# Performance work log

Measured on AMD Instinct MI355X. Metric: run time of the kernel, lower is better.

The kernel has to match this reference:

```python
import jax, jax.numpy as jnp
import numpy as np

H, W = 512, 512
CHUNK = 128            # gaussians blended per scan step
BLUR = 0.3             # antialiasing dilation (as in 3DGS EWA low-pass)
ALPHA_MIN = 1.0 / 255.0
ALPHA_MAX = 0.99


def setup_inputs() -> dict:
    key = jax.random.key(0)
    k = jax.random.split(key, 6)
    N = 8192
    means2D = jax.random.uniform(k[0], (N, 2), jnp.float32) * jnp.array([W, H], jnp.float32)
    colors = jax.random.uniform(k[1], (N, 3), jnp.float32)
    opacities = jax.random.uniform(k[2], (N, 1), jnp.float32)
    scales = jax.random.uniform(k[3], (N, 2), jnp.float32) * 15.0 + 1.0   # pixels
    rotations = jax.random.uniform(k[4], (N, 1), jnp.float32) * (2.0 * np.pi)
    depths = jax.random.uniform(k[5], (N,), jnp.float32)
    background = jnp.zeros((3,), jnp.float32)
    return dict(means2D=means2D, colors=colors, opacities=opacities,
                scales=scales, rotations=rotations, depths=depths,
                background=background)


def _rasterize(means2D, colors, opacities, scales, rotations, depths, background):
    # depth sort: front (small depth) first
    order = jnp.argsort(depths)
    m = means2D[order]                 # [N,2] (x,y)
    col = colors[order]                # [N,3]
    op = opacities[order][:, 0]        # [N]
    s = scales[order]                  # [N,2]
    th = rotations[order][:, 0]        # [N]

    # 2D covariance  Sigma = R diag(s^2) R^T
    c, si = jnp.cos(th), jnp.sin(th)
    sx2, sy2 = s[:, 0] ** 2, s[:, 1] ** 2
    A = c * c * sx2 + si * si * sy2
    Cc = si * si * sx2 + c * c * sy2
    B = c * si * (sx2 - sy2)
    det = A * Cc - B * B
    # antialiasing: dilate covariance, compensate opacity
    A2, C2 = A + BLUR, Cc + BLUR
    det2 = A2 * C2 - B * B
    op = op * jnp.sqrt(jnp.maximum(det / det2, 0.0))
    invdet = 1.0 / det2
    ia, ib, ic = C2 * invdet, -B * invdet, A2 * invdet   # Sigma^-1 entries

    # pixel centers
    ys, xs = jnp.meshgrid(jnp.arange(H, dtype=jnp.float32) + 0.5,
                          jnp.arange(W, dtype=jnp.float32) + 0.5, indexing='ij')

    N = m.shape[0]
    nchunk = N // CHUNK
    chunk = lambda a: a.reshape((nchunk, CHUNK) + a.shape[1:])
    gs = (chunk(m), chunk(col), chunk(op), chunk(ia), chunk(ib), chunk(ic))

    def step(carry, g):
        T, acc = carry                       # T:[H,W] transmittance, acc:[3,H,W]
        gm, gcol, gop, gia, gib, gic = g     # per-chunk [C,...]
        dx = xs[None] - gm[:, 0, None, None]                 # [C,H,W]
        dy = ys[None] - gm[:, 1, None, None]
        power = (-0.5 * (gia[:, None, None] * dx * dx + gic[:, None, None] * dy * dy)
                 - gib[:, None, None] * dx * dy)
        alpha = jnp.minimum(ALPHA_MAX, gop[:, None, None] * jnp.exp(power))
        alpha = jnp.where(alpha < ALPHA_MIN, 0.0, alpha)     # skip tiny splats (as CUDA)
        one_m = 1.0 - alpha
        cum = jnp.cumprod(one_m, axis=0)                     # inclusive
        Twithin = jnp.concatenate([jnp.ones_like(cum[:1]), cum[:-1]], 0)  # exclusive
        w = alpha * Twithin * T[None]                        # blend weight per gaussian
        acc = acc + jnp.einsum('nc,nhw->chw', gcol, w)
        T = T * cum[-1]
        return (T, acc), None

    init = (jnp.ones((H, W), jnp.float32), jnp.zeros((3, H, W), jnp.float32))
    (T, acc), _ = jax.lax.scan(step, init, gs)
    color = acc + background[:, None, None] * T[None]        # [3,H,W]
    return color


def reference(means2D, colors, opacities, scales, rotations, depths, background):
    return _rasterize(means2D, colors, opacities, scales, rotations, depths, background)
```

## Files before the change

kernel.cpp:

```cpp
#include <hip/hip_runtime.h>
#include <hip/hip_fp16.h>
#include <stdint.h>

#define HH 512
#define WW 512
#define NPIX (HH*WW)
#define ALPHA_MIN_C (1.0f/255.0f)
#define ALPHA_MAX_C 0.99f
#define BLUR_C 0.3f
#define TERM_EPS 1.0e-4f
#define LOG2E 1.4426950408889634f

#define JSL 512
__global__ __launch_bounds__(256) void rank_kernel(const float* __restrict__ depths,
                                                   int N, int* __restrict__ partial) {
    __shared__ uint32_t sk[JSL];
    const int tid = threadIdx.x;
    const int ngb = N >> 8;
    const int gb = blockIdx.x % ngb;
    const int jb = blockIdx.x / ngb;
    const int j0 = jb * JSL;
    for (int i = tid; i < JSL; i += 256)
        sk[i] = __float_as_uint(depths[j0 + i]);
    __syncthreads();
    const int g = gb * 256 + tid;
    const uint32_t mb = __float_as_uint(depths[g]);
    const int glim = g - j0;
    int cnt = 0;
    const uint4* sk4 = (const uint4*)sk;
#pragma unroll 8
    for (int q = 0; q < JSL / 4; ++q) {
        uint4 v = sk4[q];
        const int i4 = q * 4;
        cnt += (v.x < mb) || (v.x == mb && (i4 + 0) < glim);
        cnt += (v.y < mb) || (v.y == mb && (i4 + 1) < glim);
        cnt += (v.z < mb) || (v.z == mb && (i4 + 2) < glim);
        cnt += (v.w < mb) || (v.w == mb && (i4 + 3) < glim);
    }
    partial[jb * N + g] = cnt;
}

__global__ __launch_bounds__(256) void prep_kernel(
    const float* __restrict__ means, const float* __restrict__ colors,
    const float* __restrict__ ops, const float* __restrict__ scales,
    const float* __restrict__ rots, const int* __restrict__ partial, int N,
    float4* __restrict__ pP, float4* __restrict__ pQ) {
    int g = blockIdx.x * 256 + threadIdx.x;
    if (g >= N) return;
    int pos = 0;
#pragma unroll
    for (int s = 0; s < 16; ++s) pos += partial[s * N + g];
    float mx = means[2*g], my = means[2*g+1];
    float th = rots[g];
    float c = cosf(th), si = sinf(th);
    float sx = scales[2*g], sy = scales[2*g+1];
    float sx2 = sx*sx, sy2 = sy*sy;
    float A  = c*c*sx2 + si*si*sy2;
    float Cc = si*si*sx2 + c*c*sy2;
    float B  = c*si*(sx2 - sy2);
    float det = A*Cc - B*B;
    float A2 = A + BLUR_C, C2 = Cc + BLUR_C;
    float det2 = A2*C2 - B*B;
    float op = ops[g] * sqrtf(fmaxf(det/det2, 0.0f));
    float invd = 1.0f/det2;
    float ia = C2*invd, ib = -B*invd, ic = A2*invd;
    float iaF = -0.5f*LOG2E*ia, icF = -0.5f*LOG2E*ic, ibF = -LOG2E*ib;
    float bx, by, lop;
    if (op < ALPHA_MIN_C) {
        bx = -1.0f; by = -1.0f; lop = -128.0f;
    } else {
        float t = __logf(op * 255.0f);
        bx = sqrtf(fmaxf(2.0f * t * A2, 0.0f)) * 1.0001f + 0.1f;
        by = sqrtf(fmaxf(2.0f * t * C2, 0.0f)) * 1.0001f + 0.1f;
        lop = __log2f(op);
    }
    __half2 h2 = __floats2half2_rn(ibF, icF);
    unsigned ibic; __builtin_memcpy(&ibic, &h2, 4);
    unsigned r10 = __float2uint_rn(fminf(colors[3*g  ], 1.0f) * 1023.0f);
    unsigned g10 = __float2uint_rn(fminf(colors[3*g+1], 1.0f) * 1023.0f);
    unsigned b10 = __float2uint_rn(fminf(colors[3*g+2], 1.0f) * 1023.0f);
    unsigned rgb = r10 | (g10 << 10) | (b10 << 20);
    pP[pos] = make_float4(mx, my, bx, by);
    pQ[pos] = make_float4(iaF, __uint_as_float(ibic), __uint_as_float(rgb), lop);
}

#define NSEG 8
#define SEGG 1024
#define CHK  128
#define NCHK (SEGG/CHK)

__device__ __forceinline__ uint2 packAT(float r, float g, float b, float t) {
    __half2 hrg = __floats2half2_rn(r, g);
    __half2 hbt = __floats2half2_rn(b, t);
    uint2 u;
    __builtin_memcpy(&u.x, &hrg, 4);
    __builtin_memcpy(&u.y, &hbt, 4);
    return u;
}

__global__ __launch_bounds__(64) void seg_blend_kernel(
    const float4* __restrict__ pP, const float4* __restrict__ pQ,
    uint2* __restrict__ segbuf) {
    __shared__ __align__(16) float sG[2][CHK*8];
    const int lane = threadIdx.x;
    const int tile = blockIdx.x & 1023;
    const int seg  = blockIdx.x >> 10;
    const int tX = tile & 31, tY = tile >> 5;
    const int px = tX*16 + (lane & 15);
    const int py = tY*16 + (lane >> 4);
    const float fx = px + 0.5f, fy = py + 0.5f;
    const float x0 = tX*16 + 0.5f, x1 = x0 + 15.0f;
    const float y0 = tY*16 + 0.5f, y1 = y0 + 15.0f;
    const uint64_t lm = (1ull << lane) - 1ull;
    float T0=1.f,T1=1.f,T2=1.f,T3=1.f;
    float aR0=0.f,aG0=0.f,aB0=0.f;
    float aR1=0.f,aG1=0.f,aB1=0.f;
    float aR2=0.f,aG2=0.f,aB2=0.f;
    float aR3=0.f,aG3=0.f,aB3=0.f;
    const int gb = seg * SEGG;

    float4 a0 = pP[gb+lane],    q0 = pQ[gb+lane];
    float4 a1 = pP[gb+64+lane], q1 = pQ[gb+64+lane];
    int cntA = 0, cntB = 0;
    {
        float nx = fabsf(fminf(fmaxf(a0.x,x0),x1)-a0.x);
        float ny = fabsf(fminf(fmaxf(a0.y,y0),y1)-a0.y);
        bool f0 = (nx <= a0.z) & (ny <= a0.w);
        nx = fabsf(fminf(fmaxf(a1.x,x0),x1)-a1.x);
        ny = fabsf(fminf(fmaxf(a1.y,y0),y1)-a1.y);
        bool f1 = (nx <= a1.z) & (ny <= a1.w);
        uint64_t m0 = __ballot(f0);
        if (f0) { float* rec = &sG[0][__popcll(m0 & lm)*8];
                  *(float4*)rec = make_float4(a0.x,a0.y,q0.x,q0.y);
                  *(float2*)(rec+4) = make_float2(q0.w,q0.z); }
        int c0 = (int)__popcll(m0);
        uint64_t m1 = __ballot(f1);
        if (f1) { float* rec = &sG[0][(c0 + __popcll(m1 & lm))*8];
                  *(float4*)rec = make_float4(a1.x,a1.y,q1.x,q1.y);
                  *(float2*)(rec+4) = make_float2(q1.w,q1.z); }
        cntA = c0 + (int)__popcll(m1);
    }
    {   const int g = gb + CHK + lane;
        a0 = pP[g]; q0 = pQ[g]; a1 = pP[g+64]; q1 = pQ[g+64]; }

    int cur = 0;
    for (int k = 0; k < NCHK; ++k) {
        const int nxt = cur ^ 1;
        if (k + 1 < NCHK) {
            float nx = fabsf(fminf(fmaxf(a0.x,x0),x1)-a0.x);
            float ny = fabsf(fminf(fmaxf(a0.y,y0),y1)-a0.y);
            bool f0 = (nx <= a0.z) & (ny <= a0.w);
            nx = fabsf(fminf(fmaxf(a1.x,x0),x1)-a1.x);
            ny = fabsf(fminf(fmaxf(a1.y,y0),y1)-a1.y);
            bool f1 = (nx <= a1.z) & (ny <= a1.w);
            uint64_t m0 = __ballot(f0);
            if (f0) { float* rec = &sG[nxt][__popcll(m0 & lm)*8];
                      *(float4*)rec = make_float4(a0.x,a0.y,q0.x,q0.y);
                      *(float2*)(rec+4) = make_float2(q0.w,q0.z); }
            int c0 = (int)__popcll(m0);
            uint64_t m1 = __ballot(f1);
            if (f1) { float* rec = &sG[nxt][(c0 + __popcll(m1 & lm))*8];
                      *(float4*)rec = make_float4(a1.x,a1.y,q1.x,q1.y);
                      *(float2*)(rec+4) = make_float2(q1.w,q1.z); }
            const int cn = c0 + (int)__popcll(m1);
            if (nxt == 0) cntA = cn; else cntB = cn;
            if (k + 2 < NCHK) {
                const int g = gb + (k+2)*CHK + lane;
                a0 = pP[g]; q0 = pQ[g]; a1 = pP[g+64]; q1 = pQ[g+64];
            }
        }
        const int cnt = (cur == 0) ? cntA : cntB;
        const float* segp = sG[cur];
#pragma unroll 2
        for (int i = 0; i < cnt; ++i) {
            const float4 r0 = *(const float4*)(segp + i*8);
            const float2 r1 = *(const float2*)(segp + i*8 + 4);
            float dx = fx - r0.x;
            float dy = fy - r0.y;
            unsigned hh = __float_as_uint(r0.w);
            __half2 h2; __builtin_memcpy(&h2, &hh, 4);
            float ibv = __half2float(h2.x);
            float icv = __half2float(h2.y);
            float bse = fmaf(r0.z, dx*dx, r1.x);
            float pb  = ibv * dx;
            float d1 = dy + 4.0f, d2 = dy + 8.0f, d3 = dy + 12.0f;
            float p0 = fmaf(icv, dy*dy, fmaf(pb, dy, bse));
            float p1 = fmaf(icv, d1*d1, fmaf(pb, d1, bse));
            float p2 = fmaf(icv, d2*d2, fmaf(pb, d2, bse));
            float p3 = fmaf(icv, d3*d3, fmaf(pb, d3, bse));
            float al0 = fminf(ALPHA_MAX_C, exp2f(p0));
            float al1 = fminf(ALPHA_MAX_C, exp2f(p1));
            float al2 = fminf(ALPHA_MAX_C, exp2f(p2));
            float al3 = fminf(ALPHA_MAX_C, exp2f(p3));
            al0 = (al0 >= ALPHA_MIN_C) ? al0 : 0.0f;
            al1 = (al1 >= ALPHA_MIN_C) ? al1 : 0.0f;
            al2 = (al2 >= ALPHA_MIN_C) ? al2 : 0.0f;
            al3 = (al3 >= ALPHA_MIN_C) ? al3 : 0.0f;
            if (__any((al0 > 0.f) | (al1 > 0.f) | (al2 > 0.f) | (al3 > 0.f))) {
                unsigned rgb = __float_as_uint(r1.y);
                float cr = (float)(rgb & 1023u)         * (1.0f/1023.0f);
                float cg = (float)((rgb >> 10) & 1023u) * (1.0f/1023.0f);
                float cb = (float)((rgb >> 20) & 1023u) * (1.0f/1023.0f);
                float s0 = al0*T0, s1 = al1*T1, s2 = al2*T2, s3 = al3*T3;
                aR0 = fmaf(cr,s0,aR0); aG0 = fmaf(cg,s0,aG0); aB0 = fmaf(cb,s0,aB0);
                aR1 = fmaf(cr,s1,aR1); aG1 = fmaf(cg,s1,aG1); aB1 = fmaf(cb,s1,aB1);
                aR2 = fmaf(cr,s2,aR2); aG2 = fmaf(cg,s2,aG2); aB2 = fmaf(cb,s2,aB2);
                aR3 = fmaf(cr,s3,aR3); aG3 = fmaf(cg,s3,aG3); aB3 = fmaf(cb,s3,aB3);
                T0 = fmaf(-al0,T0,T0); T1 = fmaf(-al1,T1,T1);
                T2 = fmaf(-al2,T2,T2); T3 = fmaf(-al3,T3,T3);
            }
        }
        if (__all((T0 < TERM_EPS) & (T1 < TERM_EPS) &
                  (T2 < TERM_EPS) & (T3 < TERM_EPS))) break;
        cur = nxt;
    }
    const int pix0 = py*WW + px;
    uint2* sb = segbuf + seg * NPIX;
    sb[pix0        ] = packAT(aR0, aG0, aB0, T0);
    sb[pix0 +  4*WW] = packAT(aR1, aG1, aB1, T1);
    sb[pix0 +  8*WW] = packAT(aR2, aG2, aB2, T2);
    sb[pix0 + 12*WW] = packAT(aR3, aG3, aB3, T3);
}

__global__ __launch_bounds__(256) void composite_kernel(
    const uint2* __restrict__ segbuf, const float* __restrict__ bg,
    float* __restrict__ out) {
    const int pix = blockIdx.x * 256 + threadIdx.x;
    float R = 0.f, G = 0.f, B = 0.f, T = 1.f;
#pragma unroll
    for (int s = 0; s < NSEG; ++s) {
        uint2 v = segbuf[s * NPIX + pix];
        __half2 hrg, hbt;
        __builtin_memcpy(&hrg, &v.x, 4);
        __builtin_memcpy(&hbt, &v.y, 4);
        R = fmaf(T, __half2float(hrg.x), R);
        G = fmaf(T, __half2float(hrg.y), G);
        B = fmaf(T, __half2float(hbt.x), B);
        T *= __half2float(hbt.y);
    }
    out[pix]          = R + bg[0]*T;
    out[pix +   NPIX] = G + bg[1]*T;
    out[pix + 2*NPIX] = B + bg[2]*T;
}

extern "C" void kernel_launch(void* const* d_in, const int* in_sizes, int n_in,
                              void* d_out, int out_size, void* d_ws, size_t ws_size,
                              hipStream_t stream) {
    const float* means   = (const float*)d_in[0];
    const float* colors  = (const float*)d_in[1];
    const float* ops     = (const float*)d_in[2];
    const float* scales  = (const float*)d_in[3];
    const float* rots    = (const float*)d_in[4];
    const float* depths  = (const float*)d_in[5];
    const float* bg      = (const float*)d_in[6];
    const int N = in_sizes[0] / 2;

    char* ws = (char*)d_ws;
    float4* pP    = (float4*)(ws);
    float4* pQ    = (float4*)(ws + (size_t)N*16);
    int*    part  = (int*)  (ws + (size_t)N*32);
    uint2*  segb  = (uint2*)(ws + (size_t)N*32 + (size_t)16*N*4);

    const int ngb = N / 256;
    const int njb = N / JSL;
    rank_kernel<<<dim3(ngb*njb), dim3(256), 0, stream>>>(depths, N, part);
    prep_kernel<<<dim3((N+255)/256), dim3(256), 0, stream>>>(
        means, colors, ops, scales, rots, part, N, pP, pQ);
    seg_blend_kernel<<<dim3(NSEG*1024), dim3(64), 0, stream>>>(pP, pQ, segb);
    composite_kernel<<<dim3(NPIX/256), dim3(256), 0, stream>>>(
        segb, bg, (float*)d_out);
}
```

Before: 133.4 us.

## Store colors as fp16/fp32 instead of 10-bit packed; pack two segments per block

Colors are no longer quantised to 10-bit packed integers. Red and green are stored as a half2 and blue as a separate fp32 array, so the blend loop does not have to unpack and rescale them. The blend kernel now runs two 64-thread waves per block, each handling a different depth segment of the same tile, with separate shared buffers per wave. This halves the grid size and probably aims to improve accuracy and cut decode ALU work, in exchange for an extra global load stream and larger shared records.

```diff
diff --git a/kernel.cpp b/kernel.cpp
--- a/kernel.cpp
+++ b/kernel.cpp
@@ -44,7 +44,7 @@
     const float* __restrict__ means, const float* __restrict__ colors,
     const float* __restrict__ ops, const float* __restrict__ scales,
     const float* __restrict__ rots, const int* __restrict__ partial, int N,
-    float4* __restrict__ pP, float4* __restrict__ pQ) {
+    float4* __restrict__ pP, float4* __restrict__ pQ, float* __restrict__ pC) {
     int g = blockIdx.x * 256 + threadIdx.x;
     if (g >= N) return;
     int pos = 0;
@@ -76,12 +76,11 @@
     }
     __half2 h2 = __floats2half2_rn(ibF, icF);
     unsigned ibic; __builtin_memcpy(&ibic, &h2, 4);
-    unsigned r10 = __float2uint_rn(fminf(colors[3*g  ], 1.0f) * 1023.0f);
-    unsigned g10 = __float2uint_rn(fminf(colors[3*g+1], 1.0f) * 1023.0f);
-    unsigned b10 = __float2uint_rn(fminf(colors[3*g+2], 1.0f) * 1023.0f);
-    unsigned rgb = r10 | (g10 << 10) | (b10 << 20);
+    __half2 cc = __floats2half2_rn(colors[3*g], colors[3*g+1]);
+    unsigned crcg; __builtin_memcpy(&crcg, &cc, 4);
     pP[pos] = make_float4(mx, my, bx, by);
-    pQ[pos] = make_float4(iaF, __uint_as_float(ibic), __uint_as_float(rgb), lop);
+    pQ[pos] = make_float4(iaF, __uint_as_float(ibic), lop, __uint_as_float(crcg));
+    pC[pos] = colors[3*g+2];
 }
 
 #define NSEG 8
@@ -98,13 +97,15 @@
     return u;
 }
 
-__global__ __launch_bounds__(64) void seg_blend_kernel(
+__global__ __launch_bounds__(128) void seg_blend_kernel(
     const float4* __restrict__ pP, const float4* __restrict__ pQ,
-    uint2* __restrict__ segbuf) {
-    __shared__ __align__(16) float sG[2][CHK*8];
-    const int lane = threadIdx.x;
+    const float* __restrict__ pC, uint2* __restrict__ segbuf) {
+    __shared__ __align__(16) float sG[2][2][CHK*8];
+    const int tid  = threadIdx.x;
+    const int lane = tid & 63;
+    const int wid  = tid >> 6;
     const int tile = blockIdx.x & 1023;
-    const int seg  = blockIdx.x >> 10;
+    const int seg  = ((int)blockIdx.x >> 10) * 2 + wid;
     const int tX = tile & 31, tY = tile >> 5;
     const int px = tX*16 + (lane & 15);
     const int py = tY*16 + (lane >> 4);
@@ -119,8 +120,8 @@
     float aR3=0.f,aG3=0.f,aB3=0.f;
     const int gb = seg * SEGG;
 
-    float4 a0 = pP[gb+lane],    q0 = pQ[gb+lane];
-    float4 a1 = pP[gb+64+lane], q1 = pQ[gb+64+lane];
+    float4 a0 = pP[gb+lane],    q0 = pQ[gb+lane];    float c0f = pC[gb+lane];
+    float4 a1 = pP[gb+64+lane], q1 = pQ[gb+64+lane]; float c1f = pC[gb+64+lane];
     int cntA = 0, cntB = 0;
     {
         float nx = fabsf(fminf(fmaxf(a0.x,x0),x1)-a0.x);
@@ -130,18 +131,19 @@
         ny = fabsf(fminf(fmaxf(a1.y,y0),y1)-a1.y);
         bool f1 = (nx <= a1.z) & (ny <= a1.w);
         uint64_t m0 = __ballot(f0);
-        if (f0) { float* rec = &sG[0][__popcll(m0 & lm)*8];
+        if (f0) { float* rec = &sG[wid][0][__popcll(m0 & lm)*8];
                   *(float4*)rec = make_float4(a0.x,a0.y,q0.x,q0.y);
-                  *(float2*)(rec+4) = make_float2(q0.w,q0.z); }
+                  *(float4*)(rec+4) = make_float4(q0.z,q0.w,c0f,0.f); }
         int c0 = (int)__popcll(m0);
         uint64_t m1 = __ballot(f1);
-        if (f1) { float* rec = &sG[0][(c0 + __popcll(m1 & lm))*8];
+        if (f1) { float* rec = &sG[wid][0][(c0 + __popcll(m1 & lm))*8];
                   *(float4*)rec = make_float4(a1.x,a1.y,q1.x,q1.y);
-                  *(float2*)(rec+4) = make_float2(q1.w,q1.z); }
+                  *(float4*)(rec+4) = make_float4(q1.z,q1.w,c1f,0.f); }
         cntA = c0 + (int)__popcll(m1);
     }
     {   const int g = gb + CHK + lane;
-        a0 = pP[g]; q0 = pQ[g]; a1 = pP[g+64]; q1 = pQ[g+64]; }
+        a0 = pP[g]; q0 = pQ[g]; c0f = pC[g];
+        a1 = pP[g+64]; q1 = pQ[g+64]; c1f = pC[g+64]; }
 
     int cur = 0;
     for (int k = 0; k < NCHK; ++k) {
@@ -154,27 +156,28 @@
             ny = fabsf(fminf(fmaxf(a1.y,y0),y1)-a1.y);
             bool f1 = (nx <= a1.z) & (ny <= a1.w);
             uint64_t m0 = __ballot(f0);
-            if (f0) { float* rec = &sG[nxt][__popcll(m0 & lm)*8];
+            if (f0) { float* rec = &sG[wid][nxt][__popcll(m0 & lm)*8];
                       *(float4*)rec = make_float4(a0.x,a0.y,q0.x,q0.y);
-                      *(float2*)(rec+4) = make_float2(q0.w,q0.z); }
+                      *(float4*)(rec+4) = make_float4(q0.z,q0.w,c0f,0.f); }
             int c0 = (int)__popcll(m0);
             uint64_t m1 = __ballot(f1);
-            if (f1) { float* rec = &sG[nxt][(c0 + __popcll(m1 & lm))*8];
+            if (f1) { float* rec = &sG[wid][nxt][(c0 + __popcll(m1 & lm))*8];
                       *(float4*)rec = make_float4(a1.x,a1.y,q1.x,q1.y);
-                      *(float2*)(rec+4) = make_float2(q1.w,q1.z); }
+                      *(float4*)(rec+4) = make_float4(q1.z,q1.w,c1f,0.f); }
             const int cn = c0 + (int)__popcll(m1);
             if (nxt == 0) cntA = cn; else cntB = cn;
             if (k + 2 < NCHK) {
                 const int g = gb + (k+2)*CHK + lane;
-                a0 = pP[g]; q0 = pQ[g]; a1 = pP[g+64]; q1 = pQ[g+64];
+                a0 = pP[g]; q0 = pQ[g]; c0f = pC[g];
+                a1 = pP[g+64]; q1 = pQ[g+64]; c1f = pC[g+64];
             }
         }
         const int cnt = (cur == 0) ? cntA : cntB;
-        const float* segp = sG[cur];
+        const float* segp = sG[wid][cur];
 #pragma unroll 2
         for (int i = 0; i < cnt; ++i) {
             const float4 r0 = *(const float4*)(segp + i*8);
-            const float2 r1 = *(const float2*)(segp + i*8 + 4);
+            const float4 r1 = *(const float4*)(segp + i*8 + 4);
             float dx = fx - r0.x;
             float dy = fy - r0.y;
             unsigned hh = __float_as_uint(r0.w);
@@ -197,10 +200,11 @@
             al2 = (al2 >= ALPHA_MIN_C) ? al2 : 0.0f;
             al3 = (al3 >= ALPHA_MIN_C) ? al3 : 0.0f;
             if (__any((al0 > 0.f) | (al1 > 0.f) | (al2 > 0.f) | (al3 > 0.f))) {
-                unsigned rgb = __float_as_uint(r1.y);
-                float cr = (float)(rgb & 1023u)         * (1.0f/1023.0f);
-                float cg = (float)((rgb >> 10) & 1023u) * (1.0f/1023.0f);
-                float cb = (float)((rgb >> 20) & 1023u) * (1.0f/1023.0f);
+                unsigned cu = __float_as_uint(r1.y);
+                __half2 ch; __builtin_memcpy(&ch, &cu, 4);
+                float cr = __half2float(ch.x);
+                float cg = __half2float(ch.y);
+                float cb = r1.z;
                 float s0 = al0*T0, s1 = al1*T1, s2 = al2*T2, s3 = al3*T3;
                 aR0 = fmaf(cr,s0,aR0); aG0 = fmaf(cg,s0,aG0); aB0 = fmaf(cb,s0,aB0);
                 aR1 = fmaf(cr,s1,aR1); aG1 = fmaf(cg,s1,aG1); aB1 = fmaf(cb,s1,aB1);
@@ -258,15 +262,16 @@
     char* ws = (char*)d_ws;
     float4* pP    = (float4*)(ws);
     float4* pQ    = (float4*)(ws + (size_t)N*16);
-    int*    part  = (int*)  (ws + (size_t)N*32);
-    uint2*  segb  = (uint2*)(ws + (size_t)N*32 + (size_t)16*N*4);
+    float*  pC    = (float*) (ws + (size_t)N*32);
+    int*    part  = (int*)  (ws + (size_t)N*36);
+    uint2*  segb  = (uint2*)(ws + (size_t)N*36 + (size_t)16*N*4);
 
     const int ngb = N / 256;
     const int njb = N / JSL;
     rank_kernel<<<dim3(ngb*njb), dim3(256), 0, stream>>>(depths, N, part);
     prep_kernel<<<dim3((N+255)/256), dim3(256), 0, stream>>>(
-        means, colors, ops, scales, rots, part, N, pP, pQ);
-    seg_blend_kernel<<<dim3(NSEG*1024), dim3(64), 0, stream>>>(pP, pQ, segb);
+        means, colors, ops, scales, rots, part, N, pP, pQ, pC);
+    seg_blend_kernel<<<dim3(4*1024), dim3(128), 0, stream>>>(pP, pQ, pC, segb);
     composite_kernel<<<dim3(NPIX/256), dim3(256), 0, stream>>>(
         segb, bg, (float*)d_out);
 }
```

Measured after the change: 132.5 us. Within noise of the previous version (-0.7%).
